# Kernel tuning notes

Measured on AMD Instinct MI355X. Metric: run time of the kernel, lower is better.

Reference implementation:

```python
import jax, jax.numpy as jnp
import numpy as np

B, L, DIM = 2, 2048, 2048
N_HEADS, N_KV_HEADS = 32, 8
HEAD_DIM = DIM // N_HEADS  # 64
SCALE = HEAD_DIM ** -0.5


def setup_inputs() -> dict:
    key = jax.random.key(0)
    ks = jax.random.split(key, 6)
    s = 0.02
    x = jax.random.normal(ks[0], (B, L, DIM), dtype=jnp.float32)
    wq = jax.random.normal(ks[1], (N_HEADS * HEAD_DIM, DIM), dtype=jnp.float32) * s
    wk = jax.random.normal(ks[2], (N_KV_HEADS * HEAD_DIM, DIM), dtype=jnp.float32) * s
    wv = jax.random.normal(ks[3], (N_KV_HEADS * HEAD_DIM, DIM), dtype=jnp.float32) * s
    wo = jax.random.normal(ks[4], (DIM, N_HEADS * HEAD_DIM), dtype=jnp.float32) * s
    # standard RoPE frequencies: theta = 10000^(-2i/d), angle = pos * theta
    inv_freq = 1.0 / (10000.0 ** (jnp.arange(0, HEAD_DIM, 2, dtype=jnp.float32) / HEAD_DIM))
    angles = jnp.arange(L, dtype=jnp.float32)[:, None] * inv_freq[None, :]  # [L, HEAD_DIM//2]
    freqs_cos = jnp.cos(angles)
    freqs_sin = jnp.sin(angles)
    # additive causal mask [1, 1, L, L]
    causal = jnp.tril(jnp.ones((L, L), dtype=bool))
    mask = jnp.where(causal, 0.0, -1e9).astype(jnp.float32)[None, None]
    return {"x": x, "wq": wq, "wk": wk, "wv": wv, "wo": wo,
            "freqs_cos": freqs_cos, "freqs_sin": freqs_sin, "mask": mask}


def _apply_rope(t, cos, sin):
    # t: [B, H, L, D]; complex pairing is (even, odd) interleaved along D
    te, to = t[..., 0::2], t[..., 1::2]
    cos = cos[None, None, : t.shape[2], :]
    sin = sin[None, None, : t.shape[2], :]
    re = te * cos - to * sin
    im = te * sin + to * cos
    return jnp.stack([re, im], axis=-1).reshape(t.shape)


def reference(x, wq, wk, wv, wo, freqs_cos, freqs_sin, mask):
    b, l, _ = x.shape
    q = (x @ wq.T).reshape(b, l, N_HEADS, HEAD_DIM).transpose(0, 2, 1, 3)
    k = (x @ wk.T).reshape(b, l, N_KV_HEADS, HEAD_DIM).transpose(0, 2, 1, 3)
    v = (x @ wv.T).reshape(b, l, N_KV_HEADS, HEAD_DIM).transpose(0, 2, 1, 3)
    q = _apply_rope(q, freqs_cos, freqs_sin)
    k = _apply_rope(k, freqs_cos, freqs_sin)
    repeats = N_HEADS // N_KV_HEADS
    k = jnp.repeat(k, repeats, axis=1)
    v = jnp.repeat(v, repeats, axis=1)
    scores = jnp.einsum("bhqd,bhkd->bhqk", q, k) * SCALE + mask
    probs = jax.nn.softmax(scores, axis=-1)
    out = jnp.einsum("bhqk,bhkd->bhqd", probs, v)
    out = out.transpose(0, 2, 1, 3).reshape(b, l, N_HEADS * HEAD_DIM)
    return out @ wo.T
```

## Files before the change

### kernel.cpp

```cpp
#include <hip/hip_runtime.h>
#include <hip/hip_bf16.h>
#include <stdint.h>

typedef __attribute__((ext_vector_type(8))) short bf16x8;
typedef __attribute__((ext_vector_type(4))) float f32x4;
typedef __attribute__((ext_vector_type(16))) float f32x16;
typedef __attribute__((ext_vector_type(4))) unsigned int u32x4;

#define B_    2
#define L_    2048
#define DIM_  2048
#define NH_   32
#define NKV_  8
#define HD_   64
#define KVD_  512
#define CLOG_ 0.1803368801111244f

__device__ __forceinline__ unsigned short f2bf(float f) {
  unsigned u = __float_as_uint(f);
  u += 0x7fff + ((u >> 16) & 1);
  return (unsigned short)(u >> 16);
}
__device__ __forceinline__ unsigned cvtpk(float lo, float hi_) {
  unsigned r;
  asm("v_cvt_pk_bf16_f32 %0, %1, %2" : "=v"(r) : "v"(lo), "v"(hi_));
  return r;
}

#define GLDS16(gsrc, ldst) __builtin_amdgcn_global_load_lds( \
    (const __attribute__((address_space(1))) unsigned int*)(gsrc), \
    (__attribute__((address_space(3))) unsigned int*)(ldst), 16, 0, 0)

__global__ void cvt_all(const float* __restrict__ x,  const float* __restrict__ wq,
                        const float* __restrict__ wk, const float* __restrict__ wv,
                        const float* __restrict__ wo,
                        unsigned short* __restrict__ xb,  unsigned short* __restrict__ wqb,
                        unsigned short* __restrict__ wkb, unsigned short* __restrict__ wvb,
                        unsigned short* __restrict__ wob) {
  int i = blockIdx.x * blockDim.x + threadIdx.x;
  const float* src; unsigned short* dst; int off;
  if (i < 2097152)      { src = x;  dst = xb;  off = i; }
  else if (i < 3145728) { src = wq; dst = wqb; off = i - 2097152; }
  else if (i < 3407872) { src = wk; dst = wkb; off = i - 3145728; }
  else if (i < 3670016) { src = wv; dst = wvb; off = i - 3407872; }
  else                  { src = wo; dst = wob; off = i - 3670016; }
  float4 v = reinterpret_cast<const float4*>(src)[off];
  ushort4 o;
  o.x = f2bf(v.x); o.y = f2bf(v.y); o.z = f2bf(v.z); o.w = f2bf(v.w);
  reinterpret_cast<ushort4*>(dst)[off] = o;
}

template<int OUT_F32>
__global__ __launch_bounds__(256) void gemm_bt(
    const unsigned short* __restrict__ A,
    const unsigned short* __restrict__ W,
    void* __restrict__ C, int M, int N, int K)
{
  __shared__ unsigned short As[128 * 64];
  __shared__ unsigned short Bs[128 * 64];
  const int tid = threadIdx.x;
  const int lane = tid & 63, wid = tid >> 6;
  const int wm = wid >> 1, wn = wid & 1;
  const int r = lane & 15, g = lane >> 4;
  const int m0 = blockIdx.y * 128, n0 = blockIdx.x * 128;
  f32x4 acc[4][4] = {};
  for (int k0 = 0; k0 < K; k0 += 64) {
#pragma unroll
    for (int p = 0; p < 4; ++p) {
      int off = (p * 256 + tid) * 16;
      int row = off >> 7, colb = off & 127;
      GLDS16((const char*)A + ((size_t)(m0 + row) * K + k0) * 2 + colb,
             (char*)As + off);
      GLDS16((const char*)W + ((size_t)(n0 + row) * K + k0) * 2 + colb,
             (char*)Bs + off);
    }
    __syncthreads();
#pragma unroll
    for (int kk = 0; kk < 2; ++kk) {
      bf16x8 af[4], bfv[4];
#pragma unroll
      for (int i = 0; i < 4; ++i)
        af[i] = *reinterpret_cast<const bf16x8*>(&As[(wm * 64 + i * 16 + r) * 64 + kk * 32 + g * 8]);
#pragma unroll
      for (int i = 0; i < 4; ++i)
        bfv[i] = *reinterpret_cast<const bf16x8*>(&Bs[(wn * 64 + i * 16 + r) * 64 + kk * 32 + g * 8]);
#pragma unroll
      for (int i = 0; i < 4; ++i)
#pragma unroll
        for (int j = 0; j < 4; ++j)
          acc[i][j] = __builtin_amdgcn_mfma_f32_16x16x32_bf16(af[i], bfv[j], acc[i][j], 0, 0, 0);
    }
    __syncthreads();
  }
#pragma unroll
  for (int i = 0; i < 4; ++i)
#pragma unroll
    for (int jf = 0; jf < 4; ++jf)
#pragma unroll
      for (int j = 0; j < 4; ++j) {
        size_t row = (size_t)(m0 + wm * 64 + i * 16 + g * 4 + j);
        size_t col = (size_t)(n0 + wn * 64 + jf * 16 + r);
        float v = acc[i][jf][j];
        if (OUT_F32) ((float*)C)[row * N + col] = v;
        else ((unsigned short*)C)[row * N + col] = f2bf(v);
      }
}

__global__ __launch_bounds__(256) void gemm_qkv(
    const unsigned short* __restrict__ A,
    const unsigned short* __restrict__ Wq,
    const unsigned short* __restrict__ Wk,
    const unsigned short* __restrict__ Wv,
    unsigned short* __restrict__ Cq,
    unsigned short* __restrict__ Ck,
    unsigned short* __restrict__ Cv)
{
  __shared__ unsigned short As[128 * 64];
  __shared__ unsigned short Bs[128 * 64];
  const int tid = threadIdx.x;
  const int lane = tid & 63, wid = tid >> 6;
  const int wm = wid >> 1, wn = wid & 1;
  const int r = lane & 15, g = lane >> 4;
  const int bx = blockIdx.x;
  const unsigned short* W; unsigned short* C; int N, n0;
  if (bx < 16)      { W = Wq; C = Cq; N = 2048; n0 = bx * 128; }
  else if (bx < 20) { W = Wk; C = Ck; N = 512;  n0 = (bx - 16) * 128; }
  else              { W = Wv; C = Cv; N = 512;  n0 = (bx - 20) * 128; }
  const int m0 = blockIdx.y * 128;
  const int K = DIM_;
  f32x4 acc[4][4] = {};
  for (int k0 = 0; k0 < K; k0 += 64) {
#pragma unroll
    for (int p = 0; p < 4; ++p) {
      int off = (p * 256 + tid) * 16;
      int row = off >> 7, colb = off & 127;
      GLDS16((const char*)A + ((size_t)(m0 + row) * K + k0) * 2 + colb,
             (char*)As + off);
      GLDS16((const char*)W + ((size_t)(n0 + row) * K + k0) * 2 + colb,
             (char*)Bs + off);
    }
    __syncthreads();
#pragma unroll
    for (int kk = 0; kk < 2; ++kk) {
      bf16x8 af[4], bfv[4];
#pragma unroll
      for (int i = 0; i < 4; ++i)
        af[i] = *reinterpret_cast<const bf16x8*>(&As[(wm * 64 + i * 16 + r) * 64 + kk * 32 + g * 8]);
#pragma unroll
      for (int i = 0; i < 4; ++i)
        bfv[i] = *reinterpret_cast<const bf16x8*>(&Bs[(wn * 64 + i * 16 + r) * 64 + kk * 32 + g * 8]);
#pragma unroll
      for (int i = 0; i < 4; ++i)
#pragma unroll
        for (int j = 0; j < 4; ++j)
          acc[i][j] = __builtin_amdgcn_mfma_f32_16x16x32_bf16(af[i], bfv[j], acc[i][j], 0, 0, 0);
    }
    __syncthreads();
  }
#pragma unroll
  for (int i = 0; i < 4; ++i)
#pragma unroll
    for (int jf = 0; jf < 4; ++jf)
#pragma unroll
      for (int j = 0; j < 4; ++j) {
        size_t row = (size_t)(m0 + wm * 64 + i * 16 + g * 4 + j);
        size_t col = (size_t)(n0 + wn * 64 + jf * 16 + r);
        C[row * N + col] = f2bf(acc[i][jf][j]);
      }
}

__global__ void rope_kernel(unsigned short* __restrict__ t,
                            const float* __restrict__ fc,
                            const float* __restrict__ fs, int rowElems,
                            float scale) {
  int p = blockIdx.x * blockDim.x + threadIdx.x;
  int pairsPerRow = rowElems >> 1;
  int row = p / pairsPerRow;
  if (row >= B_ * L_) return;
  int pi = p - row * pairsPerRow;
  int l = row & (L_ - 1);
  int h = pi >> 5, i = pi & 31;
  size_t base = (size_t)row * rowElems + h * 64 + 2 * i;
  float te = __uint_as_float(((unsigned)t[base]) << 16);
  float to = __uint_as_float(((unsigned)t[base + 1]) << 16);
  float c = fc[l * 32 + i] * scale, s = fs[l * 32 + i] * scale;
  t[base]     = f2bf(te * c - to * s);
  t[base + 1] = f2bf(te * s + to * c);
}

__global__ void transpose_v(const unsigned short* __restrict__ V,
                            unsigned short* __restrict__ Vt) {
  __shared__ unsigned short tile[64][65];
  int bkv = blockIdx.y;
  int b = bkv >> 3, kv = bkv & 7;
  int l0 = blockIdx.x * 64;
  int t = threadIdx.x;
#pragma unroll
  for (int it = 0; it < 16; ++it) {
    int idx = it * 256 + t;
    int lr = idx >> 6, dc = idx & 63;
    tile[lr][dc] = V[((size_t)(b * L_) + l0 + lr) * KVD_ + kv * HD_ + dc];
  }
  __syncthreads();
#pragma unroll
  for (int it = 0; it < 16; ++it) {
    int idx = it * 256 + t;
    int dr = idx >> 6, lc = idx & 63;
    Vt[(((size_t)(b * NKV_ + kv)) * HD_ + dr) * L_ + l0 + lc] = tile[lc][dr];
  }
}

__global__ __launch_bounds__(256) void attn_kernel(
    const unsigned short* __restrict__ Q,
    const unsigned short* __restrict__ K,
    const unsigned short* __restrict__ Vt,
    unsigned short* __restrict__ AO)
{
  __shared__ unsigned short Ks[2][64 * 64];
  __shared__ unsigned short Vs[2][64 * 64];
  const int tid = threadIdx.x;
  const int lane = tid & 63, w = tid >> 6;
  const int ql = lane & 31;
  const int hi = lane >> 5;
  const int wid = blockIdx.x;
  const int j = wid >> 6;
  const int blk = j >> 2, pos = j & 3;
  const int base = 15 - 4 * blk;
  const int qt = (blk & 1) ? (base - 3 + pos) : (base - pos);
  const int bh = wid & 63;
  const int b = bh >> 5, h = bh & 31, kv = h >> 2;
  const int q0 = qt * 128;
  const int qw = q0 + w * 32;
  const int nkt = (q0 + 128) >> 6;

  bf16x8 qf[4];
  const unsigned short* qbase = Q + ((size_t)(b * L_ + qw + ql)) * DIM_ + h * HD_ + hi * 8;
#pragma unroll
  for (int dk = 0; dk < 4; ++dk)
    qf[dk] = *reinterpret_cast<const bf16x8*>(qbase + dk * 16);

  const unsigned short* Kg = K + (size_t)b * L_ * KVD_ + kv * HD_;
  const unsigned short* Vg = Vt + ((size_t)(b * NKV_ + kv)) * HD_ * L_;

  f32x16 oacc0 = {}, oacc1 = {};
  float lrow = 0.f;
  const int rsw = (ql & 7) << 4;

  auto STAGE = [&](int buf, int t) {
    const int k0 = t * 64;
#pragma unroll
    for (int p = 0; p < 2; ++p) {
      int off = (p * 256 + tid) * 16;
      int row = off >> 7;
      int colb = (off & 127) ^ ((row & 7) << 4);
      GLDS16((const char*)Kg + ((size_t)(k0 + row)) * (KVD_ * 2) + colb,
             (char*)Ks[buf] + off);
      GLDS16((const char*)Vg + ((size_t)row) * (L_ * 2) + (size_t)k0 * 2 + colb,
             (char*)Vs[buf] + off);
    }
  };

  int cur = 0;
  STAGE(0, 0);
  __syncthreads();

  for (int t = 0; t < nkt; ++t) {
    if (t + 1 < nkt) STAGE(cur ^ 1, t + 1);
    const int k0 = t * 64;
    if (k0 < qw + 32) {
      const char* Kl = (const char*)Ks[cur];
      const char* Vl = (const char*)Vs[cur];
      f32x16 s0 = {}, s1 = {};
      __builtin_amdgcn_s_setprio(1);
#pragma unroll
      for (int dk = 0; dk < 4; ++dk) {
        bf16x8 kf0 = *reinterpret_cast<const bf16x8*>(Kl + ql * 128 + ((dk * 32 + hi * 16) ^ rsw));
        bf16x8 kf1 = *reinterpret_cast<const bf16x8*>(Kl + (32 + ql) * 128 + ((dk * 32 + hi * 16) ^ rsw));
        s0 = __builtin_amdgcn_mfma_f32_32x32x16_bf16(kf0, qf[dk], s0, 0, 0, 0);
        s1 = __builtin_amdgcn_mfma_f32_32x32x16_bf16(kf1, qf[dk], s1, 0, 0, 0);
      }
      __builtin_amdgcn_s_setprio(0);
      float p[32];
      float ps = 0.f;
      if (k0 + 63 > qw) {
        int q = qw + ql;
#pragma unroll
        for (int i = 0; i < 32; ++i) {
          float sv = (i < 16) ? s0[i] : s1[i - 16];
          int kk = k0 + (i >> 4) * 32 + (i & 3) + 8 * ((i & 15) >> 2) + 4 * hi;
          float e = exp2f(sv);
          e = (kk > q) ? 0.f : e;
          p[i] = e; ps += e;
        }
      } else {
#pragma unroll
        for (int i = 0; i < 32; ++i) {
          float sv = (i < 16) ? s0[i] : s1[i - 16];
          p[i] = exp2f(sv); ps += p[i];
        }
      }
      ps += __shfl_xor(ps, 32);
      lrow += ps;
      bf16x8 pf[4];
#pragma unroll
      for (int s = 0; s < 4; ++s) {
        int bp = ((s >> 1) << 4) + ((s & 1) << 3);
        unsigned w0 = cvtpk(p[bp + 0], p[bp + 1]);
        unsigned w1 = cvtpk(p[bp + 2], p[bp + 3]);
        unsigned w2 = cvtpk(p[bp + 4], p[bp + 5]);
        unsigned w3 = cvtpk(p[bp + 6], p[bp + 7]);
        unsigned x0 = (unsigned)__shfl_xor((int)w0, 32);
        unsigned x1 = (unsigned)__shfl_xor((int)w1, 32);
        unsigned x2 = (unsigned)__shfl_xor((int)w2, 32);
        unsigned x3 = (unsigned)__shfl_xor((int)w3, 32);
        u32x4 fw;
        fw[0] = hi ? x2 : w0;
        fw[1] = hi ? x3 : w1;
        fw[2] = hi ? w2 : x0;
        fw[3] = hi ? w3 : x1;
        pf[s] = __builtin_bit_cast(bf16x8, fw);
      }
      __builtin_amdgcn_s_setprio(1);
#pragma unroll
      for (int s = 0; s < 4; ++s) {
        bf16x8 v0 = *reinterpret_cast<const bf16x8*>(Vl + ql * 128 + ((s * 32 + hi * 16) ^ rsw));
        bf16x8 v1 = *reinterpret_cast<const bf16x8*>(Vl + (32 + ql) * 128 + ((s * 32 + hi * 16) ^ rsw));
        oacc0 = __builtin_amdgcn_mfma_f32_32x32x16_bf16(v0, pf[s], oacc0, 0, 0, 0);
        oacc1 = __builtin_amdgcn_mfma_f32_32x32x16_bf16(v1, pf[s], oacc1, 0, 0, 0);
      }
      __builtin_amdgcn_s_setprio(0);
    }
    __syncthreads();
    cur ^= 1;
  }

  float inv = 1.f / lrow;
  unsigned short* obase = AO + ((size_t)(b * L_ + qw + ql)) * DIM_ + h * HD_;
#pragma unroll
  for (int g4 = 0; g4 < 4; ++g4) {
    uint2 u;
    u.x = cvtpk(oacc0[g4 * 4 + 0] * inv, oacc0[g4 * 4 + 1] * inv);
    u.y = cvtpk(oacc0[g4 * 4 + 2] * inv, oacc0[g4 * 4 + 3] * inv);
    *reinterpret_cast<uint2*>(obase + g4 * 8 + hi * 4) = u;
    uint2 v;
    v.x = cvtpk(oacc1[g4 * 4 + 0] * inv, oacc1[g4 * 4 + 1] * inv);
    v.y = cvtpk(oacc1[g4 * 4 + 2] * inv, oacc1[g4 * 4 + 3] * inv);
    *reinterpret_cast<uint2*>(obase + 32 + g4 * 8 + hi * 4) = v;
  }
}

extern "C" void kernel_launch(void* const* d_in, const int* in_sizes, int n_in,
                              void* d_out, int out_size, void* d_ws, size_t ws_size,
                              hipStream_t stream) {
  const float* x  = (const float*)d_in[0];
  const float* wq = (const float*)d_in[1];
  const float* wk = (const float*)d_in[2];
  const float* wv = (const float*)d_in[3];
  const float* wo = (const float*)d_in[4];
  const float* fc = (const float*)d_in[5];
  const float* fs = (const float*)d_in[6];
  float* out = (float*)d_out;

  unsigned short* ws  = (unsigned short*)d_ws;
  unsigned short* xb  = ws;
  unsigned short* wqb = xb  + 8388608;
  unsigned short* wkb = wqb + 4194304;
  unsigned short* wvb = wkb + 1048576;
  unsigned short* wob = wvb + 1048576;
  unsigned short* Qb  = wob + 4194304;
  unsigned short* Kb  = Qb  + 8388608;
  unsigned short* Vb  = Kb  + 2097152;
  unsigned short* Vtb = Vb  + 2097152;
  unsigned short* AOb = Vtb + 2097152;

  cvt_all<<<18432, 256, 0, stream>>>(x, wq, wk, wv, wo, xb, wqb, wkb, wvb, wob);

  gemm_qkv<<<dim3(24, 32), 256, 0, stream>>>(xb, wqb, wkb, wvb, Qb, Kb, Vb);

  rope_kernel<<<16384, 256, 0, stream>>>(Qb, fc, fs, 2048, CLOG_);
  rope_kernel<<<4096,  256, 0, stream>>>(Kb, fc, fs, 512, 1.0f);

  transpose_v<<<dim3(32, 16), 256, 0, stream>>>(Vb, Vtb);

  attn_kernel<<<1024, 256, 0, stream>>>(Qb, Kb, Vtb, AOb);

  gemm_bt<1><<<dim3(16, 32), 256, 0, stream>>>(AOb, wob, out, 4096, 2048, 2048);
}
```

Before: 256.9 us.

## Double-buffer GEMM LDS tiles, fuse V transpose into QKV epilogue, vectorize RoPE

Both GEMM kernels now use two LDS buffers and prefetch the next K-tile while computing the current one, so global loads overlap the MFMA work. The QKV GEMM writes V straight into the transposed layout with packed bf16 stores, which removes the separate transpose kernel and one intermediate buffer. RoPE is rewritten to process 8 bf16 values per thread with vector loads and stores. LDS use per block doubles, which may reduce occupancy.

```diff
diff --git a/kernel.cpp b/kernel.cpp
--- a/kernel.cpp
+++ b/kernel.cpp
@@ -25,6 +25,9 @@
   unsigned r;
   asm("v_cvt_pk_bf16_f32 %0, %1, %2" : "=v"(r) : "v"(lo), "v"(hi_));
   return r;
+}
+__device__ __forceinline__ float bf2f(unsigned short h) {
+  return __uint_as_float(((unsigned)h) << 16);
 }
 
 #define GLDS16(gsrc, ldst) __builtin_amdgcn_global_load_lds( \
@@ -56,34 +59,42 @@
     const unsigned short* __restrict__ W,
     void* __restrict__ C, int M, int N, int K)
 {
-  __shared__ unsigned short As[128 * 64];
-  __shared__ unsigned short Bs[128 * 64];
+  __shared__ unsigned short As[2][128 * 64];
+  __shared__ unsigned short Bs[2][128 * 64];
   const int tid = threadIdx.x;
   const int lane = tid & 63, wid = tid >> 6;
   const int wm = wid >> 1, wn = wid & 1;
   const int r = lane & 15, g = lane >> 4;
   const int m0 = blockIdx.y * 128, n0 = blockIdx.x * 128;
   f32x4 acc[4][4] = {};
-  for (int k0 = 0; k0 < K; k0 += 64) {
+
+  auto STAGE = [&](int buf, int k0) {
 #pragma unroll
     for (int p = 0; p < 4; ++p) {
       int off = (p * 256 + tid) * 16;
       int row = off >> 7, colb = off & 127;
       GLDS16((const char*)A + ((size_t)(m0 + row) * K + k0) * 2 + colb,
-             (char*)As + off);
+             (char*)As[buf] + off);
       GLDS16((const char*)W + ((size_t)(n0 + row) * K + k0) * 2 + colb,
-             (char*)Bs + off);
-    }
-    __syncthreads();
+             (char*)Bs[buf] + off);
+    }
+  };
+
+  const int nt = K >> 6;
+  STAGE(0, 0);
+  __syncthreads();
+  int cur = 0;
+  for (int kt = 0; kt < nt; ++kt) {
+    if (kt + 1 < nt) STAGE(cur ^ 1, (kt + 1) << 6);
 #pragma unroll
     for (int kk = 0; kk < 2; ++kk) {
       bf16x8 af[4], bfv[4];
 #pragma unroll
       for (int i = 0; i < 4; ++i)
-        af[i] = *reinterpret_cast<const bf16x8*>(&As[(wm * 64 + i * 16 + r) * 64 + kk * 32 + g * 8]);
-#pragma unroll
-      for (int i = 0; i < 4; ++i)
-        bfv[i] = *reinterpret_cast<const bf16x8*>(&Bs[(wn * 64 + i * 16 + r) * 64 + kk * 32 + g * 8]);
+        af[i] = *reinterpret_cast<const bf16x8*>(&As[cur][(wm * 64 + i * 16 + r) * 64 + kk * 32 + g * 8]);
+#pragma unroll
+      for (int i = 0; i < 4; ++i)
+        bfv[i] = *reinterpret_cast<const bf16x8*>(&Bs[cur][(wn * 64 + i * 16 + r) * 64 + kk * 32 + g * 8]);
 #pragma unroll
       for (int i = 0; i < 4; ++i)
 #pragma unroll
@@ -91,6 +102,7 @@
           acc[i][j] = __builtin_amdgcn_mfma_f32_16x16x32_bf16(af[i], bfv[j], acc[i][j], 0, 0, 0);
     }
     __syncthreads();
+    cur ^= 1;
   }
 #pragma unroll
   for (int i = 0; i < 4; ++i)
@@ -113,42 +125,50 @@
     const unsigned short* __restrict__ Wv,
     unsigned short* __restrict__ Cq,
     unsigned short* __restrict__ Ck,
-    unsigned short* __restrict__ Cv)
+    unsigned short* __restrict__ Vt)
 {
-  __shared__ unsigned short As[128 * 64];
-  __shared__ unsigned short Bs[128 * 64];
+  __shared__ unsigned short As[2][128 * 64];
+  __shared__ unsigned short Bs[2][128 * 64];
   const int tid = threadIdx.x;
   const int lane = tid & 63, wid = tid >> 6;
   const int wm = wid >> 1, wn = wid & 1;
   const int r = lane & 15, g = lane >> 4;
   const int bx = blockIdx.x;
-  const unsigned short* W; unsigned short* C; int N, n0;
+  const unsigned short* W; unsigned short* C; int N, n0; bool isV = false;
   if (bx < 16)      { W = Wq; C = Cq; N = 2048; n0 = bx * 128; }
   else if (bx < 20) { W = Wk; C = Ck; N = 512;  n0 = (bx - 16) * 128; }
-  else              { W = Wv; C = Cv; N = 512;  n0 = (bx - 20) * 128; }
+  else              { W = Wv; C = Vt; N = 512;  n0 = (bx - 20) * 128; isV = true; }
   const int m0 = blockIdx.y * 128;
   const int K = DIM_;
   f32x4 acc[4][4] = {};
-  for (int k0 = 0; k0 < K; k0 += 64) {
+
+  auto STAGE = [&](int buf, int k0) {
 #pragma unroll
     for (int p = 0; p < 4; ++p) {
       int off = (p * 256 + tid) * 16;
       int row = off >> 7, colb = off & 127;
       GLDS16((const char*)A + ((size_t)(m0 + row) * K + k0) * 2 + colb,
-             (char*)As + off);
+             (char*)As[buf] + off);
       GLDS16((const char*)W + ((size_t)(n0 + row) * K + k0) * 2 + colb,
-             (char*)Bs + off);
-    }
-    __syncthreads();
+             (char*)Bs[buf] + off);
+    }
+  };
+
+  const int nt = K >> 6;
+  STAGE(0, 0);
+  __syncthreads();
+  int cur = 0;
+  for (int kt = 0; kt < nt; ++kt) {
+    if (kt + 1 < nt) STAGE(cur ^ 1, (kt + 1) << 6);
 #pragma unroll
     for (int kk = 0; kk < 2; ++kk) {
       bf16x8 af[4], bfv[4];
 #pragma unroll
       for (int i = 0; i < 4; ++i)
-        af[i] = *reinterpret_cast<const bf16x8*>(&As[(wm * 64 + i * 16 + r) * 64 + kk * 32 + g * 8]);
-#pragma unroll
-      for (int i = 0; i < 4; ++i)
-        bfv[i] = *reinterpret_cast<const bf16x8*>(&Bs[(wn * 64 + i * 16 + r) * 64 + kk * 32 + g * 8]);
+        af[i] = *reinterpret_cast<const bf16x8*>(&As[cur][(wm * 64 + i * 16 + r) * 64 + kk * 32 + g * 8]);
+#pragma unroll
+      for (int i = 0; i < 4; ++i)
+        bfv[i] = *reinterpret_cast<const bf16x8*>(&Bs[cur][(wn * 64 + i * 16 + r) * 64 + kk * 32 + g * 8]);
 #pragma unroll
       for (int i = 0; i < 4; ++i)
 #pragma unroll
@@ -156,58 +176,66 @@
           acc[i][j] = __builtin_amdgcn_mfma_f32_16x16x32_bf16(af[i], bfv[j], acc[i][j], 0, 0, 0);
     }
     __syncthreads();
-  }
-#pragma unroll
-  for (int i = 0; i < 4; ++i)
-#pragma unroll
-    for (int jf = 0; jf < 4; ++jf)
-#pragma unroll
-      for (int j = 0; j < 4; ++j) {
-        size_t row = (size_t)(m0 + wm * 64 + i * 16 + g * 4 + j);
-        size_t col = (size_t)(n0 + wn * 64 + jf * 16 + r);
-        C[row * N + col] = f2bf(acc[i][jf][j]);
-      }
-}
-
-__global__ void rope_kernel(unsigned short* __restrict__ t,
-                            const float* __restrict__ fc,
-                            const float* __restrict__ fs, int rowElems,
-                            float scale) {
-  int p = blockIdx.x * blockDim.x + threadIdx.x;
-  int pairsPerRow = rowElems >> 1;
-  int row = p / pairsPerRow;
+    cur ^= 1;
+  }
+
+  if (isV) {
+#pragma unroll
+    for (int i = 0; i < 4; ++i)
+#pragma unroll
+      for (int jf = 0; jf < 4; ++jf) {
+        int col = n0 + wn * 64 + jf * 16 + r;
+        int kvi = col >> 6, d = col & 63;
+        int tok = m0 + wm * 64 + i * 16 + g * 4;
+        int bb = tok >> 11, tl = tok & (L_ - 1);
+        uint2 u;
+        u.x = cvtpk(acc[i][jf][0], acc[i][jf][1]);
+        u.y = cvtpk(acc[i][jf][2], acc[i][jf][3]);
+        *reinterpret_cast<uint2*>(Vt + ((size_t)((bb * NKV_ + kvi) * HD_ + d)) * L_ + tl) = u;
+      }
+  } else {
+#pragma unroll
+    for (int i = 0; i < 4; ++i)
+#pragma unroll
+      for (int jf = 0; jf < 4; ++jf)
+#pragma unroll
+        for (int j = 0; j < 4; ++j) {
+          size_t row = (size_t)(m0 + wm * 64 + i * 16 + g * 4 + j);
+          size_t col = (size_t)(n0 + wn * 64 + jf * 16 + r);
+          C[row * N + col] = f2bf(acc[i][jf][j]);
+        }
+  }
+}
+
+__global__ void rope_v8(unsigned short* __restrict__ t,
+                        const float* __restrict__ fc,
+                        const float* __restrict__ fs,
+                        int rowElems, int lshift, float scale) {
+  int idx = blockIdx.x * blockDim.x + threadIdx.x;
+  int row = idx >> lshift;
   if (row >= B_ * L_) return;
-  int pi = p - row * pairsPerRow;
+  int pos = (idx & ((1 << lshift) - 1)) << 3;
   int l = row & (L_ - 1);
-  int h = pi >> 5, i = pi & 31;
-  size_t base = (size_t)row * rowElems + h * 64 + 2 * i;
-  float te = __uint_as_float(((unsigned)t[base]) << 16);
-  float to = __uint_as_float(((unsigned)t[base + 1]) << 16);
-  float c = fc[l * 32 + i] * scale, s = fs[l * 32 + i] * scale;
-  t[base]     = f2bf(te * c - to * s);
-  t[base + 1] = f2bf(te * s + to * c);
-}
-
-__global__ void transpose_v(const unsigned short* __restrict__ V,
-                            unsigned short* __restrict__ Vt) {
-  __shared__ unsigned short tile[64][65];
-  int bkv = blockIdx.y;
-  int b = bkv >> 3, kv = bkv & 7;
-  int l0 = blockIdx.x * 64;
-  int t = threadIdx.x;
-#pragma unroll
-  for (int it = 0; it < 16; ++it) {
-    int idx = it * 256 + t;
-    int lr = idx >> 6, dc = idx & 63;
-    tile[lr][dc] = V[((size_t)(b * L_) + l0 + lr) * KVD_ + kv * HD_ + dc];
-  }
-  __syncthreads();
-#pragma unroll
-  for (int it = 0; it < 16; ++it) {
-    int idx = it * 256 + t;
-    int dr = idx >> 6, lc = idx & 63;
-    Vt[(((size_t)(b * NKV_ + kv)) * HD_ + dr) * L_ + l0 + lc] = tile[lc][dr];
-  }
+  int i0 = (pos & 63) >> 1;
+  unsigned short* p = t + (size_t)row * rowElems + pos;
+  uint4 v = *reinterpret_cast<const uint4*>(p);
+  float4 c4 = *reinterpret_cast<const float4*>(fc + l * 32 + i0);
+  float4 s4 = *reinterpret_cast<const float4*>(fs + l * 32 + i0);
+  float cc[4] = {c4.x * scale, c4.y * scale, c4.z * scale, c4.w * scale};
+  float ss[4] = {s4.x * scale, s4.y * scale, s4.z * scale, s4.w * scale};
+  unsigned wds[4] = {v.x, v.y, v.z, v.w};
+  uint4 o;
+  unsigned ow[4];
+#pragma unroll
+  for (int k = 0; k < 4; ++k) {
+    float te = bf2f((unsigned short)(wds[k] & 0xffff));
+    float to = bf2f((unsigned short)(wds[k] >> 16));
+    float re = te * cc[k] - to * ss[k];
+    float im = te * ss[k] + to * cc[k];
+    ow[k] = cvtpk(re, im);
+  }
+  o.x = ow[0]; o.y = ow[1]; o.z = ow[2]; o.w = ow[3];
+  *reinterpret_cast<uint4*>(p) = o;
 }
 
 __global__ __launch_bounds__(256) void attn_kernel(
@@ -369,18 +397,15 @@
   unsigned short* wob = wvb + 1048576;
   unsigned short* Qb  = wob + 4194304;
   unsigned short* Kb  = Qb  + 8388608;
-  unsigned short* Vb  = Kb  + 2097152;
-  unsigned short* Vtb = Vb  + 2097152;
+  unsigned short* Vtb = Kb  + 2097152;
   unsigned short* AOb = Vtb + 2097152;
 
   cvt_all<<<18432, 256, 0, stream>>>(x, wq, wk, wv, wo, xb, wqb, wkb, wvb, wob);
 
-  gemm_qkv<<<dim3(24, 32), 256, 0, stream>>>(xb, wqb, wkb, wvb, Qb, Kb, Vb);
-
-  rope_kernel<<<16384, 256, 0, stream>>>(Qb, fc, fs, 2048, CLOG_);
-  rope_kernel<<<4096,  256, 0, stream>>>(Kb, fc, fs, 512, 1.0f);
-
-  transpose_v<<<dim3(32, 16), 256, 0, stream>>>(Vb, Vtb);
+  gemm_qkv<<<dim3(24, 32), 256, 0, stream>>>(xb, wqb, wkb, wvb, Qb, Kb, Vtb);
+
+  rope_v8<<<4096, 256, 0, stream>>>(Qb, fc, fs, 2048, 8, CLOG_);
+  rope_v8<<<1024, 256, 0, stream>>>(Kb, fc, fs, 512, 6, 1.0f);
 
   attn_kernel<<<1024, 256, 0, stream>>>(Qb, Kb, Vtb, AOb);
 
```

New measurement: 271.2 us. 5.6% more time.
